# Optimization experiments

Hardware: AMD Instinct MI355X
Metric: run time of the kernel (lower is better)

Reference implementation:

```python
import jax, jax.numpy as jnp
import numpy as np

D_MODEL = 1024
NUM_HEADS = 16
DEPTH = D_MODEL // NUM_HEADS


def setup_inputs() -> dict:
    key = jax.random.key(0)
    ks = jax.random.split(key, 11)
    B, S = 2, 2048
    s = 1.0 / np.sqrt(D_MODEL)
    return {
        "q": jax.random.normal(ks[0], (B, S, D_MODEL), jnp.float32),
        "k": jax.random.normal(ks[1], (B, S, D_MODEL), jnp.float32),
        "v": jax.random.normal(ks[2], (B, S, D_MODEL), jnp.float32),
        "wq": jax.random.normal(ks[3], (D_MODEL, D_MODEL), jnp.float32) * s,
        "bq": jax.random.normal(ks[4], (D_MODEL,), jnp.float32) * s,
        "wk": jax.random.normal(ks[5], (D_MODEL, D_MODEL), jnp.float32) * s,
        "bk": jax.random.normal(ks[6], (D_MODEL,), jnp.float32) * s,
        "wv": jax.random.normal(ks[7], (D_MODEL, D_MODEL), jnp.float32) * s,
        "bv": jax.random.normal(ks[8], (D_MODEL,), jnp.float32) * s,
        "wo": jax.random.normal(ks[9], (D_MODEL, D_MODEL), jnp.float32) * s,
        "bo": jax.random.normal(ks[10], (D_MODEL,), jnp.float32) * s,
    }


def _split_heads(x, B):
    # [B, S, D] -> [B, H, S, depth]
    return x.reshape(B, -1, NUM_HEADS, DEPTH).transpose(0, 2, 1, 3)


def reference(q, k, v, wq, bq, wk, bk, wv, bv, wo, bo):
    B, S, _ = q.shape
    # torch Linear: y = x @ W.T + b
    qh = _split_heads(q @ wq.T + bq, B)
    kh = _split_heads(k @ wk.T + bk, B)
    vh = _split_heads(v @ wv.T + bv, B)
    scale = jnp.sqrt(jnp.asarray(DEPTH, jnp.float32))
    scores = jnp.einsum("bhqd,bhkd->bhqk", qh, kh) / scale  # [B,H,S,S]
    attn = jax.nn.softmax(scores, axis=-1)
    out = jnp.einsum("bhqk,bhkd->bhqd", attn, vh)
    out = out.transpose(0, 2, 1, 3).reshape(B, S, D_MODEL)
    return out @ wo.T + bo
```

## Files before the change

### kernel.cpp

```cpp
#include <hip/hip_runtime.h>
#include <hip/hip_bf16.h>
#include <math.h>

#define D_MODEL 1024
#define NUM_HEADS 16
#define DEPTH 64
#define BATCH 2
#define SEQ 2048
#define N_TOK (BATCH * SEQ)

typedef short bf16x8 __attribute__((ext_vector_type(8)));
typedef _Float16 f16x8 __attribute__((ext_vector_type(8)));
typedef float f32x4  __attribute__((ext_vector_type(4)));
typedef unsigned short u16x8 __attribute__((ext_vector_type(8)));
typedef unsigned short u16x4 __attribute__((ext_vector_type(4)));
typedef unsigned int u32x4 __attribute__((ext_vector_type(4)));

__device__ __forceinline__ unsigned short f2b(float x) {
    return __builtin_bit_cast(unsigned short, __float2bfloat16(x));
}
__device__ __forceinline__ float b2f(unsigned short h) {
    return __builtin_bit_cast(float, (unsigned int)h << 16);
}
__device__ __forceinline__ unsigned short f2h(float x) {
    return __builtin_bit_cast(unsigned short, (_Float16)x);
}

__device__ __forceinline__ void pl32_swap(unsigned int& x, unsigned int& y) {
    auto r = __builtin_amdgcn_permlane32_swap(x, y, false, false);
    x = (unsigned int)r[0]; y = (unsigned int)r[1];
}
__device__ __forceinline__ void pl16_swap(unsigned int& x, unsigned int& y) {
    auto r = __builtin_amdgcn_permlane16_swap(x, y, false, false);
    x = (unsigned int)r[0]; y = (unsigned int)r[1];
}

__global__ __launch_bounds__(256) void prep_weights(
    const float* __restrict__ s0, const float* __restrict__ s1,
    const float* __restrict__ s2, const float* __restrict__ s3,
    unsigned short* __restrict__ f0, unsigned short* __restrict__ f1,
    unsigned short* __restrict__ f2,
    unsigned short* __restrict__ h3, unsigned short* __restrict__ l3,
    int n8)
{
    const int i = blockIdx.x * 256 + threadIdx.x;
    if (i >= n8) return;
    const int which = blockIdx.y;
    const float* src = (which == 0) ? s0 : (which == 1) ? s1 : (which == 2) ? s2 : s3;
    const float4 a0 = ((const float4*)src)[2 * i];
    const float4 a1 = ((const float4*)src)[2 * i + 1];
    const float xs[8] = {a0.x, a0.y, a0.z, a0.w, a1.x, a1.y, a1.z, a1.w};
    if (which < 3) {
        unsigned short* dst = (which == 0) ? f0 : (which == 1) ? f1 : f2;
        u16x8 o;
        #pragma unroll
        for (int e = 0; e < 8; ++e) o[e] = f2h(xs[e]);
        *(u16x8*)&dst[(size_t)i * 8] = o;
    } else {
        u16x8 h8, l8;
        #pragma unroll
        for (int e = 0; e < 8; ++e) {
            const unsigned short h = f2b(xs[e]);
            h8[e] = h;
            l8[e] = f2b(xs[e] - b2f(h));
        }
        *(u16x8*)&h3[(size_t)i * 8] = h8;
        *(u16x8*)&l3[(size_t)i * 8] = l8;
    }
}

__global__ __launch_bounds__(256, 4) void qkv_gemm(
    const float* __restrict__ Aq, const float* __restrict__ Ak,
    const float* __restrict__ Av,
    const unsigned short* __restrict__ Wq, const unsigned short* __restrict__ Wk,
    const unsigned short* __restrict__ Wv,
    const float* __restrict__ bq, const float* __restrict__ bk,
    const float* __restrict__ bv,
    void* __restrict__ Yq, void* __restrict__ Yk, void* __restrict__ Yvp)
{
    __shared__ unsigned short sA[2][64][64];
    __shared__ unsigned short sB[2][64][64];

    const int z = blockIdx.z;
    const float* Af = (z == 0) ? Aq : (z == 1) ? Ak : Av;
    const unsigned short* Bf = (z == 0) ? Wq : (z == 1) ? Wk : Wv;
    const float* bias = (z == 0) ? bq : (z == 1) ? bk : bv;
    const float scale = (z == 0) ? 0.125f : 1.0f;
    const int mode = (z == 2) ? 2 : 1;
    void* Yv = (z == 0) ? Yq : (z == 1) ? Yk : Yvp;

    const int tid  = threadIdx.x;
    const int wave = tid >> 6;
    const int lane = tid & 63;
    const int quad = lane >> 4;
    const int l16  = lane & 15;
    const int wm   = wave >> 1;
    const int wn   = wave & 1;

    const int j0 = blockIdx.x * 64;
    const int i0 = blockIdx.y * 64;

    const int sc  = tid & 7;
    const int r32 = tid >> 3;

    f32x4 acc[2][2] = {};

    float4 fq[2][2];

    auto loadA = [&](int s) {
        const int k0 = s * 64;
        #pragma unroll
        for (int p = 0; p < 2; ++p) {
            const int row = p * 32 + r32;
            const int cg = (sc ^ (row & 7)) * 8;
            const float* srcp = &Af[(size_t)(i0 + row) * 1024 + k0 + cg];
            fq[p][0] = *(const float4*)srcp;
            fq[p][1] = *(const float4*)(srcp + 4);
        }
    };
    auto writeA = [&](int buf) {
        #pragma unroll
        for (int p = 0; p < 2; ++p) {
            const int row = p * 32 + r32;
            const float xs[8] = {fq[p][0].x, fq[p][0].y, fq[p][0].z, fq[p][0].w,
                                 fq[p][1].x, fq[p][1].y, fq[p][1].z, fq[p][1].w};
            u16x8 o;
            #pragma unroll
            for (int e = 0; e < 8; ++e) o[e] = f2h(xs[e]);
            *(u16x8*)&sA[buf][row][sc * 8] = o;
        }
    };
    auto stageB = [&](int buf, int s) {
        const int k0 = s * 64;
        #pragma unroll
        for (int p = 0; p < 2; ++p) {
            const int row = p * 32 + r32;
            const int cg = (sc ^ (row & 7)) * 8;
            __builtin_amdgcn_global_load_lds(
                (const __attribute__((address_space(1))) unsigned int*)
                    &Bf[(size_t)(j0 + row) * 1024 + k0 + cg],
                (__attribute__((address_space(3))) unsigned int*)&sB[buf][row][sc * 8],
                16, 0, 0);
        }
    };

    loadA(0);
    stageB(0, 0);
    __asm__ volatile("s_waitcnt vmcnt(0)" ::: "memory");
    writeA(0);
    __syncthreads();

    int cur = 0;
    for (int s = 0; s < 16; ++s) {
        if (s + 1 < 16) { loadA(s + 1); stageB(cur ^ 1, s + 1); }

        #pragma unroll
        for (int ks = 0; ks < 2; ++ks) {
            f16x8 a[2], b[2];
            #pragma unroll
            for (int mt = 0; mt < 2; ++mt) {
                const int row = wm * 32 + mt * 16 + l16;
                const int c = (((ks * 4 + quad) ^ (row & 7))) * 8;
                a[mt] = *(const f16x8*)&sA[cur][row][c];
            }
            #pragma unroll
            for (int nt = 0; nt < 2; ++nt) {
                const int row = wn * 32 + nt * 16 + l16;
                const int c = (((ks * 4 + quad) ^ (row & 7))) * 8;
                b[nt] = *(const f16x8*)&sB[cur][row][c];
            }
            #pragma unroll
            for (int mt = 0; mt < 2; ++mt)
                #pragma unroll
                for (int nt = 0; nt < 2; ++nt)
                    acc[mt][nt] = __builtin_amdgcn_mfma_f32_16x16x32_f16(a[mt], b[nt], acc[mt][nt], 0, 0, 0);
        }

        if (s + 1 < 16) {
            __asm__ volatile("s_waitcnt vmcnt(0)" ::: "memory");
            writeA(cur ^ 1);
        }
        __syncthreads();
        cur ^= 1;
    }

    float bvv[2];
    #pragma unroll
    for (int nt = 0; nt < 2; ++nt)
        bvv[nt] = bias[j0 + wn * 32 + nt * 16 + l16];

    #pragma unroll
    for (int mt = 0; mt < 2; ++mt) {
        const int ibase = i0 + wm * 32 + mt * 16 + quad * 4;
        #pragma unroll
        for (int nt = 0; nt < 2; ++nt) {
            const int j = j0 + wn * 32 + nt * 16 + l16;
            const int h = j >> 6, d = j & 63;
            if (mode == 1) {
                __hip_bfloat16* Y = (__hip_bfloat16*)Yv;
                #pragma unroll
                for (int r = 0; r < 4; ++r) {
                    const int i = ibase + r;
                    const int b = i >> 11, ss = i & (SEQ - 1);
                    Y[(((size_t)(b * NUM_HEADS + h) * SEQ) + ss) * DEPTH + d] =
                        __float2bfloat16((acc[mt][nt][r] + bvv[nt]) * scale);
                }
            } else {
                unsigned short* Y = (unsigned short*)Yv;
                const int b = ibase >> 11;
                u16x4 pack;
                #pragma unroll
                for (int r = 0; r < 4; ++r)
                    pack[r] = f2b((acc[mt][nt][r] + bvv[nt]) * scale);
                *(u16x4*)&Y[(((size_t)(b * NUM_HEADS + h) * DEPTH) + d) * SEQ
                            + (ibase & (SEQ - 1))] = pack;
            }
        }
    }
}

__global__ __launch_bounds__(512, 2) void gemm_bf16x3(
    const unsigned short* __restrict__ Ahi,
    const unsigned short* __restrict__ Alo,
    const unsigned short* __restrict__ Bhi,
    const unsigned short* __restrict__ Blo,
    const float* __restrict__ bias,
    float* __restrict__ Y,
    float scale)
{
    __shared__ unsigned short sAh[128][64];
    __shared__ unsigned short sAl[128][64];
    __shared__ unsigned short sBh[128][64];
    __shared__ unsigned short sBl[128][64];

    const int tid  = threadIdx.x;
    const int wave = tid >> 6;
    const int lane = tid & 63;
    const int quad = lane >> 4;
    const int l16  = lane & 15;
    const int wm   = wave >> 1;
    const int wn   = wave & 1;

    const int j0 = blockIdx.x * 128;
    const int i0 = blockIdx.y * 128;

    const int sc  = tid & 7;
    const int r64 = tid >> 3;

    u16x8 preH[4], preL[4];

    #pragma unroll
    for (int p = 0; p < 4; ++p) {
        const int row256 = p * 64 + r64;
        const bool isA = row256 < 128;
        const int row = isA ? row256 : row256 - 128;
        const unsigned short* srcH = isA ? Ahi : Bhi;
        const unsigned short* srcL = isA ? Alo : Blo;
        const int grow = (isA ? i0 : j0) + row;
        const int cg = (sc ^ (row & 7)) * 8;
        const size_t go = (size_t)grow * 1024 + cg;
        preH[p] = *(const u16x8*)&srcH[go];
        preL[p] = *(const u16x8*)&srcL[go];
    }

    f32x4 acc[2][4] = {};

    for (int s = 0; s < 16; ++s) {
        __syncthreads();

        #pragma unroll
        for (int p = 0; p < 4; ++p) {
            const int row256 = p * 64 + r64;
            const bool isA = row256 < 128;
            const int row = isA ? row256 : row256 - 128;
            unsigned short (*dh)[64] = isA ? sAh : sBh;
            unsigned short (*dl)[64] = isA ? sAl : sBl;
            *(u16x8*)&dh[row][sc * 8] = preH[p];
            *(u16x8*)&dl[row][sc * 8] = preL[p];
        }
        __syncthreads();

        if (s + 1 < 16) {
            const int k0 = (s + 1) * 64;
            #pragma unroll
            for (int p = 0; p < 4; ++p) {
                const int row256 = p * 64 + r64;
                const bool isA = row256 < 128;
                const int row = isA ? row256 : row256 - 128;
                const unsigned short* srcH = isA ? Ahi : Bhi;
                const unsigned short* srcL = isA ? Alo : Blo;
                const int grow = (isA ? i0 : j0) + row;
                const int cg = (sc ^ (row & 7)) * 8;
                const size_t go = (size_t)grow * 1024 + k0 + cg;
                preH[p] = *(const u16x8*)&srcH[go];
                preL[p] = *(const u16x8*)&srcL[go];
            }
        }

        #pragma unroll
        for (int ks = 0; ks < 2; ++ks) {
            bf16x8 ah[2], al[2], bh[4], bl[4];
            #pragma unroll
            for (int mt = 0; mt < 2; ++mt) {
                const int row = wm * 32 + mt * 16 + l16;
                const int c = (((ks * 4 + quad) ^ (row & 7))) * 8;
                ah[mt] = *(const bf16x8*)&sAh[row][c];
                al[mt] = *(const bf16x8*)&sAl[row][c];
            }
            #pragma unroll
            for (int nt = 0; nt < 4; ++nt) {
                const int row = wn * 64 + nt * 16 + l16;
                const int c = (((ks * 4 + quad) ^ (row & 7))) * 8;
                bh[nt] = *(const bf16x8*)&sBh[row][c];
                bl[nt] = *(const bf16x8*)&sBl[row][c];
            }
            #pragma unroll
            for (int mt = 0; mt < 2; ++mt)
                #pragma unroll
                for (int nt = 0; nt < 4; ++nt) {
                    acc[mt][nt] = __builtin_amdgcn_mfma_f32_16x16x32_bf16(ah[mt], bh[nt], acc[mt][nt], 0, 0, 0);
                    acc[mt][nt] = __builtin_amdgcn_mfma_f32_16x16x32_bf16(ah[mt], bl[nt], acc[mt][nt], 0, 0, 0);
                    acc[mt][nt] = __builtin_amdgcn_mfma_f32_16x16x32_bf16(al[mt], bh[nt], acc[mt][nt], 0, 0, 0);
                }
        }
    }

    float bv[4];
    #pragma unroll
    for (int nt = 0; nt < 4; ++nt)
        bv[nt] = bias[j0 + wn * 64 + nt * 16 + l16];

    #pragma unroll
    for (int mt = 0; mt < 2; ++mt) {
        const int ibase = i0 + wm * 32 + mt * 16 + quad * 4;
        #pragma unroll
        for (int nt = 0; nt < 4; ++nt) {
            const int j = j0 + wn * 64 + nt * 16 + l16;
            #pragma unroll
            for (int r = 0; r < 4; ++r)
                Y[(size_t)(ibase + r) * 1024 + j] = (acc[mt][nt][r] + bv[nt]) * scale;
        }
    }
}

__global__ __launch_bounds__(256) void flash_attn_mfma(
    const __hip_bfloat16* __restrict__ Qg,
    const __hip_bfloat16* __restrict__ Kg,
    const __hip_bfloat16* __restrict__ Vg,
    unsigned short* __restrict__ OHi,
    unsigned short* __restrict__ OLo)
{
    __shared__ unsigned short Ks[64][72];
    __shared__ unsigned short Vt[64][72];

    const int tid  = threadIdx.x;
    const int wave = tid >> 6;
    const int lane = tid & 63;
    const int quad = lane >> 4;
    const int l16  = lane & 15;

    const int bh = blockIdx.x >> 5;
    const int q0 = (blockIdx.x & 31) * 64;

    const unsigned short* Qu = (const unsigned short*)Qg + (size_t)bh * SEQ * DEPTH;
    const unsigned short* Ku = (const unsigned short*)Kg + (size_t)bh * SEQ * DEPTH;
    const unsigned short* Vu = (const unsigned short*)Vg + (size_t)bh * DEPTH * SEQ;

    const int qrow = q0 + wave * 16 + l16;
    bf16x8 qf[2];
    qf[0] = *(const bf16x8*)&Qu[(size_t)qrow * DEPTH + quad * 8];
    qf[1] = *(const bf16x8*)&Qu[(size_t)qrow * DEPTH + 32 + quad * 8];

    bf16x8 ones;
    #pragma unroll
    for (int e = 0; e < 8; ++e) ones[e] = (short)0x3F80;

    f32x4 o_acc[4] = {};
    f32x4 l_acc = {0.f, 0.f, 0.f, 0.f};

    const int srow = tid >> 3;
    const int sc8  = (tid & 7) * 8;
    u16x8 kpre[2], vpre[2];
    #pragma unroll
    for (int it = 0; it < 2; ++it) {
        const int row = it * 32 + srow;
        kpre[it] = *(const u16x8*)&Ku[(size_t)row * DEPTH + sc8];
        vpre[it] = *(const u16x8*)&Vu[(size_t)row * SEQ + sc8];
    }

    for (int t = 0; t < 32; ++t) {
        __syncthreads();

        #pragma unroll
        for (int it = 0; it < 2; ++it) {
            const int row = it * 32 + srow;
            *(u16x8*)&Ks[row][sc8] = kpre[it];
            *(u16x8*)&Vt[row][sc8] = vpre[it];
        }
        __syncthreads();

        if (t + 1 < 32) {
            const int k0 = (t + 1) * 64;
            #pragma unroll
            for (int it = 0; it < 2; ++it) {
                const int row = it * 32 + srow;
                kpre[it] = *(const u16x8*)&Ku[(size_t)(k0 + row) * DEPTH + sc8];
                vpre[it] = *(const u16x8*)&Vu[(size_t)row * SEQ + k0 + sc8];
            }
        }

        f32x4 s[4];
        #pragma unroll
        for (int nt = 0; nt < 4; ++nt) {
            s[nt] = f32x4{0.f, 0.f, 0.f, 0.f};
            bf16x8 kf0 = *(const bf16x8*)&Ks[nt * 16 + l16][quad * 8];
            s[nt] = __builtin_amdgcn_mfma_f32_16x16x32_bf16(kf0, qf[0], s[nt], 0, 0, 0);
            bf16x8 kf1 = *(const bf16x8*)&Ks[nt * 16 + l16][32 + quad * 8];
            s[nt] = __builtin_amdgcn_mfma_f32_16x16x32_bf16(kf1, qf[1], s[nt], 0, 0, 0);
        }

        unsigned int Wp[4][2];
        #pragma unroll
        for (int nt = 0; nt < 4; ++nt) {
            #pragma unroll
            for (int b = 0; b < 2; ++b) {
                const unsigned int lo = f2b(__expf(s[nt][2 * b]));
                const unsigned int hi = f2b(__expf(s[nt][2 * b + 1]));
                Wp[nt][b] = lo | (hi << 16);
            }
        }

        unsigned int pw[8];
        #pragma unroll
        for (int b = 0; b < 2; ++b) {
            unsigned int x = Wp[0][b], y = Wp[1][b];
            pl32_swap(x, y);
            pl16_swap(x, y);
            pw[b] = x; pw[2 + b] = y;
            x = Wp[2][b]; y = Wp[3][b];
            pl32_swap(x, y);
            pl16_swap(x, y);
            pw[4 + b] = x; pw[6 + b] = y;
        }
        bf16x8 pf[2];
        {
            u32x4 t0, t1;
            #pragma unroll
            for (int j = 0; j < 4; ++j) { t0[j] = pw[j]; t1[j] = pw[4 + j]; }
            pf[0] = __builtin_bit_cast(bf16x8, t0);
            pf[1] = __builtin_bit_cast(bf16x8, t1);
        }

        #pragma unroll
        for (int nt = 0; nt < 4; ++nt) {
            bf16x8 vf0 = *(const bf16x8*)&Vt[nt * 16 + l16][quad * 8];
            o_acc[nt] = __builtin_amdgcn_mfma_f32_16x16x32_bf16(pf[0], vf0, o_acc[nt], 0, 0, 0);
            bf16x8 vf1 = *(const bf16x8*)&Vt[nt * 16 + l16][32 + quad * 8];
            o_acc[nt] = __builtin_amdgcn_mfma_f32_16x16x32_bf16(pf[1], vf1, o_acc[nt], 0, 0, 0);
        }
        l_acc = __builtin_amdgcn_mfma_f32_16x16x32_bf16(pf[0], ones, l_acc, 0, 0, 0);
        l_acc = __builtin_amdgcn_mfma_f32_16x16x32_bf16(pf[1], ones, l_acc, 0, 0, 0);
    }

    const int b = bh / NUM_HEADS;
    const int h = bh % NUM_HEADS;
    #pragma unroll
    for (int r = 0; r < 4; ++r) {
        const float inv = 1.f / l_acc[r];
        const int row = q0 + wave * 16 + quad * 4 + r;
        #pragma unroll
        for (int nt = 0; nt < 4; ++nt) {
            const float o = o_acc[nt][r] * inv;
            const size_t idx = ((size_t)(b * SEQ + row)) * D_MODEL + h * DEPTH + nt * 16 + l16;
            const unsigned short hbits = f2b(o);
            OHi[idx] = hbits;
            OLo[idx] = f2b(o - b2f(hbits));
        }
    }
}

extern "C" void kernel_launch(void* const* d_in, const int* in_sizes, int n_in,
                              void* d_out, int out_size, void* d_ws, size_t ws_size,
                              hipStream_t stream) {
    const float* q  = (const float*)d_in[0];
    const float* k  = (const float*)d_in[1];
    const float* v  = (const float*)d_in[2];
    const float* wq = (const float*)d_in[3];
    const float* bq = (const float*)d_in[4];
    const float* wk = (const float*)d_in[5];
    const float* bk = (const float*)d_in[6];
    const float* wv = (const float*)d_in[7];
    const float* bv = (const float*)d_in[8];
    const float* wo = (const float*)d_in[9];
    const float* bo = (const float*)d_in[10];
    float* out = (float*)d_out;

    char* ws = (char*)d_ws;
    const size_t MB = 1024 * 1024;
    unsigned short* AoHi = (unsigned short*)(ws);
    unsigned short* AoLo = (unsigned short*)(ws + 8 * MB);
    unsigned short* WqF  = (unsigned short*)(ws + 16 * MB);
    unsigned short* WkF  = (unsigned short*)(ws + 18 * MB);
    unsigned short* WvF  = (unsigned short*)(ws + 20 * MB);
    unsigned short* WoH  = (unsigned short*)(ws + 22 * MB);
    unsigned short* WoL  = (unsigned short*)(ws + 24 * MB);
    __hip_bfloat16* Qh   = (__hip_bfloat16*)(ws + 26 * MB);
    __hip_bfloat16* Kh   = (__hip_bfloat16*)(ws + 34 * MB);
    __hip_bfloat16* Vh   = (__hip_bfloat16*)(ws + 42 * MB);

    const int nW8 = D_MODEL * D_MODEL / 8;
    dim3 sb(256);

    prep_weights<<<dim3(nW8 / 256, 4), sb, 0, stream>>>(
        wq, wk, wv, wo, WqF, WkF, WvF, WoH, WoL, nW8);

    dim3 fblk(256);
    dim3 fgrid(D_MODEL / 64, N_TOK / 64, 3);
    qkv_gemm<<<fgrid, fblk, 0, stream>>>(
        q, k, v, WqF, WkF, WvF, bq, bk, bv, Qh, Kh, (void*)Vh);

    dim3 ablk(256);
    dim3 agrid(BATCH * NUM_HEADS * (SEQ / 64));
    flash_attn_mfma<<<agrid, ablk, 0, stream>>>(Qh, Kh, Vh, AoHi, AoLo);

    dim3 oblk(512);
    dim3 ogrid(D_MODEL / 128, N_TOK / 128);
    gemm_bf16x3<<<ogrid, oblk, 0, stream>>>(AoHi, AoLo, WoH, WoL, bo, out, 1.0f);
}
```

Baseline: 272.1 us.

## Enlarge QKV GEMM tiles to 128x128 with block swizzle and single A buffer

```diff
diff --git a/kernel.cpp b/kernel.cpp
--- a/kernel.cpp
+++ b/kernel.cpp
@@ -69,7 +69,7 @@
     }
 }
 
-__global__ __launch_bounds__(256, 4) void qkv_gemm(
+__global__ __launch_bounds__(256, 3) void qkv_gemm(
     const float* __restrict__ Aq, const float* __restrict__ Ak,
     const float* __restrict__ Av,
     const unsigned short* __restrict__ Wq, const unsigned short* __restrict__ Wk,
@@ -78,16 +78,21 @@
     const float* __restrict__ bv,
     void* __restrict__ Yq, void* __restrict__ Yk, void* __restrict__ Yvp)
 {
-    __shared__ unsigned short sA[2][64][64];
-    __shared__ unsigned short sB[2][64][64];
-
-    const int z = blockIdx.z;
-    const float* Af = (z == 0) ? Aq : (z == 1) ? Ak : Av;
-    const unsigned short* Bf = (z == 0) ? Wq : (z == 1) ? Wk : Wv;
-    const float* bias = (z == 0) ? bq : (z == 1) ? bk : bv;
-    const float scale = (z == 0) ? 0.125f : 1.0f;
-    const int mode = (z == 2) ? 2 : 1;
-    void* Yv = (z == 0) ? Yq : (z == 1) ? Yk : Yvp;
+    __shared__ unsigned short sA[128][64];
+    __shared__ unsigned short sB[2][128][64];
+
+    const int flat = (blockIdx.z * 32 + blockIdx.y) * 8 + blockIdx.x;
+    const int swz  = (flat & 7) * 96 + (flat >> 3);
+    const int bx = swz & 7;
+    const int by = (swz >> 3) & 31;
+    const int bz = swz >> 8;
+
+    const float* Af = (bz == 0) ? Aq : (bz == 1) ? Ak : Av;
+    const unsigned short* Bf = (bz == 0) ? Wq : (bz == 1) ? Wk : Wv;
+    const float* bias = (bz == 0) ? bq : (bz == 1) ? bk : bv;
+    const float scale = (bz == 0) ? 0.125f : 1.0f;
+    const int mode = (bz == 2) ? 2 : 1;
+    void* Yv = (bz == 0) ? Yq : (bz == 1) ? Yk : Yvp;
 
     const int tid  = threadIdx.x;
     const int wave = tid >> 6;
@@ -97,20 +102,20 @@
     const int wm   = wave >> 1;
     const int wn   = wave & 1;
 
-    const int j0 = blockIdx.x * 64;
-    const int i0 = blockIdx.y * 64;
+    const int j0 = bx * 128;
+    const int i0 = by * 128;
 
     const int sc  = tid & 7;
     const int r32 = tid >> 3;
 
-    f32x4 acc[2][2] = {};
-
-    float4 fq[2][2];
+    f32x4 acc[4][4] = {};
+
+    float4 fq[4][2];
 
     auto loadA = [&](int s) {
         const int k0 = s * 64;
         #pragma unroll
-        for (int p = 0; p < 2; ++p) {
+        for (int p = 0; p < 4; ++p) {
             const int row = p * 32 + r32;
             const int cg = (sc ^ (row & 7)) * 8;
             const float* srcp = &Af[(size_t)(i0 + row) * 1024 + k0 + cg];
@@ -118,22 +123,22 @@
             fq[p][1] = *(const float4*)(srcp + 4);
         }
     };
-    auto writeA = [&](int buf) {
-        #pragma unroll
-        for (int p = 0; p < 2; ++p) {
+    auto writeA = [&]() {
+        #pragma unroll
+        for (int p = 0; p < 4; ++p) {
             const int row = p * 32 + r32;
             const float xs[8] = {fq[p][0].x, fq[p][0].y, fq[p][0].z, fq[p][0].w,
                                  fq[p][1].x, fq[p][1].y, fq[p][1].z, fq[p][1].w};
             u16x8 o;
             #pragma unroll
             for (int e = 0; e < 8; ++e) o[e] = f2h(xs[e]);
-            *(u16x8*)&sA[buf][row][sc * 8] = o;
+            *(u16x8*)&sA[row][sc * 8] = o;
         }
     };
     auto stageB = [&](int buf, int s) {
         const int k0 = s * 64;
         #pragma unroll
-        for (int p = 0; p < 2; ++p) {
+        for (int p = 0; p < 4; ++p) {
             const int row = p * 32 + r32;
             const int cg = (sc ^ (row & 7)) * 8;
             __builtin_amdgcn_global_load_lds(
@@ -146,8 +151,8 @@
 
     loadA(0);
     stageB(0, 0);
+    writeA();
     __asm__ volatile("s_waitcnt vmcnt(0)" ::: "memory");
-    writeA(0);
     __syncthreads();
 
     int cur = 0;
@@ -156,45 +161,46 @@
 
         #pragma unroll
         for (int ks = 0; ks < 2; ++ks) {
-            f16x8 a[2], b[2];
-            #pragma unroll
-            for (int mt = 0; mt < 2; ++mt) {
-                const int row = wm * 32 + mt * 16 + l16;
+            f16x8 a[4], b[4];
+            #pragma unroll
+            for (int mt = 0; mt < 4; ++mt) {
+                const int row = wm * 64 + mt * 16 + l16;
                 const int c = (((ks * 4 + quad) ^ (row & 7))) * 8;
-                a[mt] = *(const f16x8*)&sA[cur][row][c];
-            }
-            #pragma unroll
-            for (int nt = 0; nt < 2; ++nt) {
-                const int row = wn * 32 + nt * 16 + l16;
+                a[mt] = *(const f16x8*)&sA[row][c];
+            }
+            #pragma unroll
+            for (int nt = 0; nt < 4; ++nt) {
+                const int row = wn * 64 + nt * 16 + l16;
                 const int c = (((ks * 4 + quad) ^ (row & 7))) * 8;
                 b[nt] = *(const f16x8*)&sB[cur][row][c];
             }
             #pragma unroll
-            for (int mt = 0; mt < 2; ++mt)
+            for (int mt = 0; mt < 4; ++mt)
                 #pragma unroll
-                for (int nt = 0; nt < 2; ++nt)
+                for (int nt = 0; nt < 4; ++nt)
                     acc[mt][nt] = __builtin_amdgcn_mfma_f32_16x16x32_f16(a[mt], b[nt], acc[mt][nt], 0, 0, 0);
         }
 
+        __syncthreads();
         if (s + 1 < 16) {
+            writeA();
             __asm__ volatile("s_waitcnt vmcnt(0)" ::: "memory");
-            writeA(cur ^ 1);
         }
         __syncthreads();
         cur ^= 1;
     }
 
-    float bvv[2];
-    #pragma unroll
-    for (int nt = 0; nt < 2; ++nt)
-        bvv[nt] = bias[j0 + wn * 32 + nt * 16 + l16];
-
-    #pragma unroll
-    for (int mt = 0; mt < 2; ++mt) {
-        const int ibase = i0 + wm * 32 + mt * 16 + quad * 4;
-        #pragma unroll
-        for (int nt = 0; nt < 2; ++nt) {
-            const int j = j0 + wn * 32 + nt * 16 + l16;
+    float bvv[4];
+    #pragma unroll
+    for (int nt = 0; nt < 4; ++nt)
+        bvv[nt] = bias[j0 + wn * 64 + nt * 16 + l16];
+
+    #pragma unroll
+    for (int mt = 0; mt < 4; ++mt) {
+        const int ibase = i0 + wm * 64 + mt * 16 + quad * 4;
+        #pragma unroll
+        for (int nt = 0; nt < 4; ++nt) {
+            const int j = j0 + wn * 64 + nt * 16 + l16;
             const int h = j >> 6, d = j & 63;
             if (mode == 1) {
                 __hip_bfloat16* Y = (__hip_bfloat16*)Yv;
@@ -515,7 +521,7 @@
         wq, wk, wv, wo, WqF, WkF, WvF, WoH, WoL, nW8);
 
     dim3 fblk(256);
-    dim3 fgrid(D_MODEL / 64, N_TOK / 64, 3);
+    dim3 fgrid(D_MODEL / 128, N_TOK / 128, 3);
     qkv_gemm<<<fgrid, fblk, 0, stream>>>(
         q, k, v, WqF, WkF, WvF, bq, bk, bv, Qh, Kh, (void*)Vh);
 
```

Measured after the change: 248.2 us. 1.1x faster.
